# Optimization experiments

Hardware: AMD Instinct MI355X
Metric: run time of the kernel (lower is better)

The kernel has to match this reference:

```python
import jax, jax.numpy as jnp
import numpy as np

B, F, T, C = 128, 512, 60, 15  # batch, feature_size, timesteps, num_cameras
H1, H2 = 128, 64               # decoder hidden channels


def setup_inputs() -> dict:
    key = jax.random.key(0)
    ks = jax.random.split(key, 6)
    x = jax.random.normal(ks[0], (B, F, T), dtype=jnp.float32)
    cam = jax.random.randint(ks[1], (B,), 0, C)
    # per-camera (expert) decoder params
    W1 = jax.random.normal(ks[2], (C, F, H1, 3, 4), dtype=jnp.float32) * 0.02  # ConvT3d F->128, k=(1,3,4)
    b1 = jnp.zeros((C, H1), dtype=jnp.float32)
    W2 = jax.random.normal(ks[3], (C, H1, H2, 3, 4), dtype=jnp.float32) * 0.02  # ConvT3d 128->64, k=s=(1,3,4)
    b2 = jnp.zeros((C, H2), dtype=jnp.float32)
    W3 = jax.random.normal(ks[4], (C, H2), dtype=jnp.float32) * 0.02            # Conv3d 64->1, k=1
    b3 = jnp.zeros((C,), dtype=jnp.float32)
    return {"x": x, "cam": cam, "W1": W1, "b1": b1, "W2": W2, "b2": b2, "W3": W3, "b3": b3}


def reference(x, cam, W1, b1, W2, b2, W3, b3):
    # MoE-style dispatch: gather each sample's camera-expert weights.
    # Layer 1: transposed conv from 1x1 -> 3x4 is a pure linear map over features.
    h1 = jnp.einsum('bft,bfopq->btopq', x, W1[cam]) + b1[cam][:, None, :, None, None]
    h1 = jax.nn.relu(h1)                                # (B,T,128,3,4)
    # Layer 2: stride == kernel => non-overlapping transposed conv, out[3p+r,4q+s].
    h2 = jnp.einsum('btipq,biors->btoprqs', h1, W2[cam])  # (B,T,64,3,3,4,4)
    h2 = h2.reshape(B, T, H2, 9, 16) + b2[cam][:, None, :, None, None]
    h2 = jax.nn.relu(h2)                                # (B,T,64,9,16)
    # Layer 3: 1x1x1 conv to a single channel, then squeeze + sigmoid.
    out = jnp.einsum('btohw,bo->bthw', h2, W3[cam]) + b3[cam][:, None, None, None]
    return jax.nn.sigmoid(out)                           # (B,T,9,16)
```

## Files before the change

kernel.cpp:

```cpp
#include <hip/hip_runtime.h>
#include <hip/hip_bf16.h>
#include <cstdint>

#define B_  128
#define F_  512
#define T_  60
#define C_  15
#define H1_ 128
#define H2_ 64

typedef short short8_t __attribute__((ext_vector_type(8)));
typedef float f32x4    __attribute__((ext_vector_type(4)));

static __device__ __forceinline__ unsigned short f2bf(float f) {
    union { float f; uint32_t u; } v; v.f = f;
    uint32_t r = v.u + 0x7FFF + ((v.u >> 16) & 1);
    return (unsigned short)(r >> 16);
}

static __device__ __forceinline__ void async_cp16(const unsigned short* g, unsigned short* l) {
    __builtin_amdgcn_global_load_lds(
        (const __attribute__((address_space(1))) unsigned int*)g,
        (__attribute__((address_space(3))) unsigned int*)l, 16, 0, 0);
}

__global__ __launch_bounds__(256) void prep_misc(
    const float* __restrict__ x, const float* __restrict__ W2,
    const int* __restrict__ cam,
    unsigned short* __restrict__ xTs, unsigned short* __restrict__ W2f,
    int* __restrict__ ord)
{
    __shared__ float sm[12288];
    const int blk = blockIdx.x, tid = threadIdx.x;

    if (blk < 512) {
        float (*xs)[61] = (float(*)[61])sm;
        const int f0 = (blk & 3) * 128, b = blk >> 2;
        #pragma unroll
        for (int it = 0; it < 32; ++it) {
            int idx = tid + it * 256;
            int fl = idx >> 6, t = idx & 63;
            if (t < T_) xs[fl][t] = x[((size_t)b * F_ + f0 + fl) * T_ + t];
        }
        __syncthreads();
        #pragma unroll
        for (int it = 0; it < 8; ++it) {
            int idx = tid + it * 256;
            int t = idx >> 5, f4 = (idx & 31) * 4;
            ushort4 o;
            o.x = (t < T_) ? f2bf(xs[f4 + 0][t]) : 0;
            o.y = (t < T_) ? f2bf(xs[f4 + 1][t]) : 0;
            o.z = (t < T_) ? f2bf(xs[f4 + 2][t]) : 0;
            o.w = (t < T_) ? f2bf(xs[f4 + 3][t]) : 0;
            const int f = f0 + f4;
            const int kc = f >> 6, within = f & 63;
            const int cc = (within >> 3) ^ (t & 7), half = (within >> 2) & 1;
            *(ushort4*)(xTs + (size_t)b * 32768 + kc * 4096 + t * 64 + cc * 8 + half * 4) = o;
        }
    } else if (blk < 632) {
        float (*ls)[384] = (float(*)[384])sm;
        const int id = blk - 512;
        const int i0 = (id & 3) * 32, o0 = ((id >> 2) & 1) * 32, c = id >> 3;
        #pragma unroll
        for (int it = 0; it < 12; ++it) {
            int idx = tid + it * 256;
            int il = idx / 96, r = idx - il * 96;
            float4 v = *(const float4*)(W2 + ((size_t)(c * H1_ + i0 + il)) * (H2_ * 12)
                                           + (size_t)o0 * 12 + r * 4);
            *(float4*)&ls[il][r * 4] = v;
        }
        __syncthreads();
        const int o_l = tid >> 3, i_l = (tid & 7) * 4;
        const int o  = o0 + o_l;
        const int nt = o >> 4, l15 = o & 15;
        const int lane = l15 + 16 * ((i_l >> 3) & 3);
        const int kk  = i0 >> 5;
        const int pos = i_l & 7;
        #pragma unroll
        for (int rs = 0; rs < 12; ++rs) {
            ushort4 v;
            v.x = f2bf(ls[i_l + 0][o_l * 12 + rs]);
            v.y = f2bf(ls[i_l + 1][o_l * 12 + rs]);
            v.z = f2bf(ls[i_l + 2][o_l * 12 + rs]);
            v.w = f2bf(ls[i_l + 3][o_l * 12 + rs]);
            *(ushort4*)(W2f + ((size_t)(c * 12 + rs) * 16 + nt * 4 + kk) * 512
                            + lane * 8 + pos) = v;
        }
    } else {
        int* cs = (int*)sm;
        if (tid < B_) cs[tid] = cam[tid];
        __syncthreads();
        if (tid < B_) {
            const int cb = cs[tid];
            int rank = 0;
            #pragma unroll 16
            for (int j = 0; j < B_; ++j) {
                int cj = cs[j];
                rank += (cj < cb || (cj == cb && j < tid)) ? 1 : 0;
            }
            ord[rank] = tid;
        }
    }
}

__global__ __launch_bounds__(256) void repack_w1(const float* __restrict__ W1,
                                                 unsigned short* __restrict__ W1s) {
    __shared__ float ls[32][384];
    const int f0 = blockIdx.x * 32, i0 = blockIdx.y * 32, c = blockIdx.z;
    const int tid = threadIdx.x;
    #pragma unroll
    for (int it = 0; it < 12; ++it) {
        int idx = tid + it * 256;
        int fl = idx / 96, r = idx - fl * 96;
        float4 v = *(const float4*)(W1 + ((size_t)(c * F_ + f0 + fl)) * (H1_ * 12)
                                       + (size_t)i0 * 12 + r * 4);
        *(float4*)&ls[fl][r * 4] = v;
    }
    __syncthreads();
    const int i_l = tid >> 3, f_l = (tid & 7) * 4;
    const int i = i0 + i_l, f = f0 + f_l;
    const int kc = f >> 6, within = f & 63;
    const int cc = (within >> 3) ^ (i & 7), half = (within >> 2) & 1;
    #pragma unroll
    for (int pq = 0; pq < 12; ++pq) {
        ushort4 o;
        o.x = f2bf(ls[f_l + 0][i_l * 12 + pq]);
        o.y = f2bf(ls[f_l + 1][i_l * 12 + pq]);
        o.z = f2bf(ls[f_l + 2][i_l * 12 + pq]);
        o.w = f2bf(ls[f_l + 3][i_l * 12 + pq]);
        *(ushort4*)(W1s + (size_t)(c * 12 + pq) * 65536
                        + kc * 8192 + i * 64 + cc * 8 + half * 4) = o;
    }
}

__global__ __launch_bounds__(256) void fused_all(
    const unsigned short* __restrict__ xTs, const unsigned short* __restrict__ W1s,
    const unsigned short* __restrict__ W2f, const int* __restrict__ cam,
    const int* __restrict__ ord,
    const float* __restrict__ b1, const float* __restrict__ b2,
    const float* __restrict__ W3, const float* __restrict__ b3,
    float* __restrict__ out)
{
    __shared__ __align__(16) unsigned short smem[24576];

    const int idx = blockIdx.x;
    const int swz = (idx & 7) * 192 + (idx >> 3);
    const int bpos = swz / 12, pq = swz - bpos * 12;
    const int b = ord[bpos];

    const int tid = threadIdx.x;
    const int w = tid >> 6, l = tid & 63;
    const int l15 = l & 15, g = l >> 4;
    const int c = cam[b];

    const unsigned short* xchunk = xTs + (size_t)b * 32768;
    const unsigned short* wchunk = W1s + (size_t)(c * 12 + pq) * 65536;

    #define STAGE1(kc, buf)                                                       \
        {                                                                         \
            _Pragma("unroll")                                                     \
            for (int k = 0; k < 2; ++k)                                           \
                async_cp16(xchunk + (kc) * 4096 + (w * 2 + k) * 512 + l * 8,      \
                           smem + (buf) * 12288 + (w * 2 + k) * 512 + l * 8);     \
            _Pragma("unroll")                                                     \
            for (int k = 0; k < 4; ++k)                                           \
                async_cp16(wchunk + (kc) * 8192 + (w * 4 + k) * 512 + l * 8,      \
                           smem + (buf) * 12288 + 4096 + (w * 4 + k) * 512 + l * 8); \
        }

    f32x4 acc1[4][2];
    #pragma unroll
    for (int mt = 0; mt < 4; ++mt) {
        acc1[mt][0] = (f32x4){0.f, 0.f, 0.f, 0.f};
        acc1[mt][1] = (f32x4){0.f, 0.f, 0.f, 0.f};
    }

    STAGE1(0, 0);
    STAGE1(1, 1);

    const int sxor = (l15 & 7);
    #pragma unroll
    for (int kc = 0; kc < 8; ++kc) {
        if (kc < 7) { asm volatile("s_waitcnt vmcnt(6)" ::: "memory"); }
        else        { asm volatile("s_waitcnt vmcnt(0)" ::: "memory"); }
        __builtin_amdgcn_s_barrier();
        asm volatile("" ::: "memory");

        const int base = (kc & 1) * 12288;
        #pragma unroll
        for (int kk2 = 0; kk2 < 2; ++kk2) {
            const int cc = (kk2 * 4 + g) ^ sxor;
            short8_t af[4], bf[2];
            #pragma unroll
            for (int mt = 0; mt < 4; ++mt)
                af[mt] = *(const short8_t*)(smem + base + (16 * mt + l15) * 64 + cc * 8);
            #pragma unroll
            for (int ni = 0; ni < 2; ++ni)
                bf[ni] = *(const short8_t*)(smem + base + 4096
                                            + (32 * w + 16 * ni + l15) * 64 + cc * 8);
            #pragma unroll
            for (int mt = 0; mt < 4; ++mt)
                #pragma unroll
                for (int ni = 0; ni < 2; ++ni)
                    acc1[mt][ni] = __builtin_amdgcn_mfma_f32_16x16x32_bf16(
                        af[mt], bf[ni], acc1[mt][ni], 0, 0, 0);
        }

        asm volatile("" ::: "memory");
        __builtin_amdgcn_s_barrier();
        if (kc < 6) STAGE1(kc + 2, kc & 1);
    }
    #undef STAGE1

    const unsigned short* W2base = W2f + (size_t)(c * 12 + w * 3) * 8192;
    short8_t bfr[2][4];
    #pragma unroll
    for (int kk = 0; kk < 4; ++kk)
        bfr[0][kk] = *(const short8_t*)(W2base + kk * 512 + l * 8);

    float w3v[4][4], b2v[4][4];
    #pragma unroll
    for (int nt = 0; nt < 4; ++nt)
        #pragma unroll
        for (int r = 0; r < 4; ++r) {
            w3v[nt][r] = W3[c * H2_ + nt * 16 + g * 4 + r];
            b2v[nt][r] = b2[c * H2_ + nt * 16 + g * 4 + r];
        }
    const float b3v = b3[c];
    const int p = pq >> 2, q = pq & 3;

    unsigned short* h1s = smem;
    #pragma unroll
    for (int ni = 0; ni < 2; ++ni) {
        const int i = 32 * w + 16 * ni + l15;
        const float b1v = b1[c * H1_ + i];
        #pragma unroll
        for (int mt = 0; mt < 4; ++mt)
            #pragma unroll
            for (int r = 0; r < 4; ++r) {
                float h = acc1[mt][ni][r] + b1v;
                h = h > 0.f ? h : 0.f;
                h1s[(16 * mt + 4 * g + r) * 136 + i] = f2bf(h);
            }
    }
    __syncthreads();

    short8_t a2[4][4];
    #pragma unroll
    for (int mt = 0; mt < 4; ++mt)
        #pragma unroll
        for (int kk = 0; kk < 4; ++kk)
            a2[mt][kk] = *(const short8_t*)&h1s[(16 * mt + l15) * 136 + 32 * kk + 8 * g];

    float s[4] = {0.f, 0.f, 0.f, 0.f};

    #pragma unroll
    for (int seg = 0; seg < 12; ++seg) {
        if (seg < 11) {
            const int ns = seg + 1;
            const unsigned short* nb = W2base + (ns >> 2) * 8192 + ((ns & 3) * 4) * 512;
            #pragma unroll
            for (int kk = 0; kk < 4; ++kk)
                bfr[(seg + 1) & 1][kk] = *(const short8_t*)(nb + kk * 512 + l * 8);
        }
        const int nt = seg & 3;
        #pragma unroll
        for (int mt = 0; mt < 4; ++mt) {
            f32x4 acc2 = (f32x4){0.f, 0.f, 0.f, 0.f};
            #pragma unroll
            for (int kk = 0; kk < 4; ++kk)
                acc2 = __builtin_amdgcn_mfma_f32_16x16x32_bf16(
                    bfr[seg & 1][kk], a2[mt][kk], acc2, 0, 0, 0);
            #pragma unroll
            for (int r = 0; r < 4; ++r)
                s[mt] = fmaf(w3v[nt][r], fmaxf(acc2[r] + b2v[nt][r], 0.f), s[mt]);
        }

        if (nt == 3) {
            const int rs = w * 3 + (seg >> 2);
            const int hrow = p * 3 + (rs >> 2), wcol = q * 4 + (rs & 3);
            #pragma unroll
            for (int mt = 0; mt < 4; ++mt) {
                s[mt] += __shfl_xor(s[mt], 16);
                s[mt] += __shfl_xor(s[mt], 32);
            }
            float v = (g & 1) ? ((g & 2) ? s[3] : s[1]) : ((g & 2) ? s[2] : s[0]);
            v += b3v;
            if (l < T_)
                out[(((size_t)b * T_ + l) * 9 + hrow) * 16 + wcol] =
                    1.f / (1.f + __expf(-v));
            s[0] = s[1] = s[2] = s[3] = 0.f;
        }
    }
}

__global__ __launch_bounds__(256) void fused_decoder_f32(
    const float* __restrict__ x,   const int* __restrict__ cam,
    const float* __restrict__ W1,  const float* __restrict__ b1,
    const float* __restrict__ W2,  const float* __restrict__ b2,
    const float* __restrict__ W3,  const float* __restrict__ b3,
    float* __restrict__ out)
{
    __shared__ float h1s[T_ * H1_];
    __shared__ float stage[8192];

    const int pq  = blockIdx.x;
    const int b   = blockIdx.y;
    const int p   = pq >> 2, q = pq & 3;
    const int tid = threadIdx.x;
    const int c   = cam[b];

    float* xs  = stage;
    float* w1s = stage + 2048;

    const int ig = tid & 31;
    const int tg = tid >> 5;

    float acc[8][4];
    #pragma unroll
    for (int a = 0; a < 8; ++a)
        #pragma unroll
        for (int j = 0; j < 4; ++j) acc[a][j] = 0.f;

    for (int f0 = 0; f0 < F_; f0 += 32) {
        __syncthreads();
        {
            int lane = tid & 63;
            int sub  = tid >> 6;
            if (lane < T_) {
                #pragma unroll
                for (int m = 0; m < 8; ++m) {
                    int kk = sub * 8 + m;
                    xs[kk * 64 + lane] = x[((size_t)b * F_ + f0 + kk) * T_ + lane];
                }
            }
        }
        for (int e = tid; e < 32 * H1_; e += 256) {
            int kk = e >> 7, i = e & 127;
            w1s[e] = W1[(((size_t)c * F_ + f0 + kk) * H1_ + i) * 12 + pq];
        }
        __syncthreads();
        #pragma unroll 8
        for (int kk = 0; kk < 32; ++kk) {
            float4 bv = *(const float4*)&w1s[kk * 128 + ig * 4];
            float4 a0 = *(const float4*)&xs[kk * 64 + tg * 8];
            float4 a1 = *(const float4*)&xs[kk * 64 + tg * 8 + 4];
            float at[8] = {a0.x, a0.y, a0.z, a0.w, a1.x, a1.y, a1.z, a1.w};
            #pragma unroll
            for (int tt = 0; tt < 8; ++tt) {
                acc[tt][0] = fmaf(at[tt], bv.x, acc[tt][0]);
                acc[tt][1] = fmaf(at[tt], bv.y, acc[tt][1]);
                acc[tt][2] = fmaf(at[tt], bv.z, acc[tt][2]);
                acc[tt][3] = fmaf(at[tt], bv.w, acc[tt][3]);
            }
        }
    }
    {
        float4 b1v = *(const float4*)&b1[c * H1_ + ig * 4];
        #pragma unroll
        for (int tt = 0; tt < 8; ++tt) {
            int t = tg * 8 + tt;
            if (t < T_) {
                float4 hv;
                hv.x = fmaxf(acc[tt][0] + b1v.x, 0.f);
                hv.y = fmaxf(acc[tt][1] + b1v.y, 0.f);
                hv.z = fmaxf(acc[tt][2] + b1v.z, 0.f);
                hv.w = fmaxf(acc[tt][3] + b1v.w, 0.f);
                *(float4*)&h1s[t * H1_ + ig * 4] = hv;
            }
        }
    }

    const int lane = tid & 63;
    const int wv   = tid >> 6;
    const float w3v = W3[c * H2_ + lane];
    const float b2v = b2[c * H2_ + lane];
    const float b3v = b3[c];
    float* w2s = stage;

    for (int rs = 0; rs < 12; ++rs) {
        __syncthreads();
        for (int e = tid; e < H1_ * H2_; e += 256) {
            int i = e >> 6, o = e & 63;
            w2s[e] = W2[(((size_t)c * H1_ + i) * H2_ + o) * 12 + rs];
        }
        __syncthreads();

        float acc2[15];
        #pragma unroll
        for (int j = 0; j < 15; ++j) acc2[j] = 0.f;

        for (int i = 0; i < H1_; i += 4) {
            float wa = w2s[(i + 0) * 64 + lane];
            float wb = w2s[(i + 1) * 64 + lane];
            float wc = w2s[(i + 2) * 64 + lane];
            float wd = w2s[(i + 3) * 64 + lane];
            #pragma unroll
            for (int j = 0; j < 15; ++j) {
                float4 h = *(const float4*)&h1s[(wv * 15 + j) * H1_ + i];
                acc2[j] = fmaf(h.x, wa, acc2[j]);
                acc2[j] = fmaf(h.y, wb, acc2[j]);
                acc2[j] = fmaf(h.z, wc, acc2[j]);
                acc2[j] = fmaf(h.w, wd, acc2[j]);
            }
        }

        const int r = rs >> 2, s = rs & 3;
        const int hrow = p * 3 + r, wcol = q * 4 + s;
        #pragma unroll
        for (int j = 0; j < 15; ++j) {
            float y = w3v * fmaxf(acc2[j] + b2v, 0.f);
            #pragma unroll
            for (int m = 32; m > 0; m >>= 1) y += __shfl_xor(y, m, 64);
            if (lane == j) {
                int t = wv * 15 + j;
                float v = y + b3v;
                out[(((size_t)b * T_ + t) * 9 + hrow) * 16 + wcol] = 1.f / (1.f + __expf(-v));
            }
        }
    }
}

extern "C" void kernel_launch(void* const* d_in, const int* in_sizes, int n_in,
                              void* d_out, int out_size, void* d_ws, size_t ws_size,
                              hipStream_t stream) {
    const float* x   = (const float*)d_in[0];
    const int*   cam = (const int*)  d_in[1];
    const float* W1  = (const float*)d_in[2];
    const float* b1  = (const float*)d_in[3];
    const float* W2  = (const float*)d_in[4];
    const float* b2  = (const float*)d_in[5];
    const float* W3  = (const float*)d_in[6];
    const float* b3  = (const float*)d_in[7];
    float* outp = (float*)d_out;

    const size_t n_xT  = (size_t)B_ * 32768;
    const size_t n_w1s = (size_t)C_ * 12 * 65536;
    const size_t n_w2f = (size_t)C_ * 12 * 16 * 512;
    const size_t needed = (n_xT + n_w1s + n_w2f) * sizeof(unsigned short)
                        + B_ * sizeof(int);

    if (d_ws != nullptr && ws_size >= needed) {
        unsigned short* xTs = (unsigned short*)d_ws;
        unsigned short* W1p = xTs + n_xT;
        unsigned short* W2p = W1p + n_w1s;
        int* ord = (int*)(W2p + n_w2f);
        prep_misc<<<633, 256, 0, stream>>>(x, W2, cam, xTs, W2p, ord);
        repack_w1<<<dim3(F_ / 32, H1_ / 32, C_), 256, 0, stream>>>(W1, W1p);
        fused_all<<<dim3(12 * B_), 256, 0, stream>>>(
            xTs, W1p, W2p, cam, ord, b1, b2, W3, b3, outp);
    } else {
        fused_decoder_f32<<<dim3(12, B_), 256, 0, stream>>>(
            x, cam, W1, b1, W2, b2, W3, b3, outp);
    }
}
```

Before: 62.75 us.

## Merge W1 repack into prep kernel and use 3-stage 32-wide K pipeline

The separate W1 repack kernel is folded into the prep kernel, saving one launch. The first-layer GEMM now uses K chunks of 32 instead of 64 with a new XOR swizzle. It keeps three LDS buffers, so one barrier per iteration can be dropped, and total shared memory goes down. The price is twice as many iterations with less work each, plus an extra sync before h1 is written into the reused LDS.

```diff
diff --git a/kernel.cpp b/kernel.cpp
--- a/kernel.cpp
+++ b/kernel.cpp
@@ -24,11 +24,13 @@
         (__attribute__((address_space(3))) unsigned int*)l, 16, 0, 0);
 }
 
-__global__ __launch_bounds__(256) void prep_misc(
+#define KEY(r) (((r) & 3) ^ (((r) >> 2) & 3))
+
+__global__ __launch_bounds__(256) void prep_all(
     const float* __restrict__ x, const float* __restrict__ W2,
-    const int* __restrict__ cam,
+    const float* __restrict__ W1, const int* __restrict__ cam,
     unsigned short* __restrict__ xTs, unsigned short* __restrict__ W2f,
-    int* __restrict__ ord)
+    unsigned short* __restrict__ W1s, int* __restrict__ ord)
 {
     __shared__ float sm[12288];
     const int blk = blockIdx.x, tid = threadIdx.x;
@@ -53,9 +55,9 @@
             o.z = (t < T_) ? f2bf(xs[f4 + 2][t]) : 0;
             o.w = (t < T_) ? f2bf(xs[f4 + 3][t]) : 0;
             const int f = f0 + f4;
-            const int kc = f >> 6, within = f & 63;
-            const int cc = (within >> 3) ^ (t & 7), half = (within >> 2) & 1;
-            *(ushort4*)(xTs + (size_t)b * 32768 + kc * 4096 + t * 64 + cc * 8 + half * 4) = o;
+            const int kc = f >> 5, kl = f & 31;
+            const int cc = (kl >> 3) ^ KEY(t);
+            *(ushort4*)(xTs + (size_t)b * 32768 + kc * 2048 + t * 32 + cc * 8 + (kl & 7)) = o;
         }
     } else if (blk < 632) {
         float (*ls)[384] = (float(*)[384])sm;
@@ -86,7 +88,7 @@
             *(ushort4*)(W2f + ((size_t)(c * 12 + rs) * 16 + nt * 4 + kk) * 512
                             + lane * 8 + pos) = v;
         }
-    } else {
+    } else if (blk == 632) {
         int* cs = (int*)sm;
         if (tid < B_) cs[tid] = cam[tid];
         __syncthreads();
@@ -100,36 +102,33 @@
             }
             ord[rank] = tid;
         }
-    }
-}
-
-__global__ __launch_bounds__(256) void repack_w1(const float* __restrict__ W1,
-                                                 unsigned short* __restrict__ W1s) {
-    __shared__ float ls[32][384];
-    const int f0 = blockIdx.x * 32, i0 = blockIdx.y * 32, c = blockIdx.z;
-    const int tid = threadIdx.x;
-    #pragma unroll
-    for (int it = 0; it < 12; ++it) {
-        int idx = tid + it * 256;
-        int fl = idx / 96, r = idx - fl * 96;
-        float4 v = *(const float4*)(W1 + ((size_t)(c * F_ + f0 + fl)) * (H1_ * 12)
-                                       + (size_t)i0 * 12 + r * 4);
-        *(float4*)&ls[fl][r * 4] = v;
-    }
-    __syncthreads();
-    const int i_l = tid >> 3, f_l = (tid & 7) * 4;
-    const int i = i0 + i_l, f = f0 + f_l;
-    const int kc = f >> 6, within = f & 63;
-    const int cc = (within >> 3) ^ (i & 7), half = (within >> 2) & 1;
-    #pragma unroll
-    for (int pq = 0; pq < 12; ++pq) {
-        ushort4 o;
-        o.x = f2bf(ls[f_l + 0][i_l * 12 + pq]);
-        o.y = f2bf(ls[f_l + 1][i_l * 12 + pq]);
-        o.z = f2bf(ls[f_l + 2][i_l * 12 + pq]);
-        o.w = f2bf(ls[f_l + 3][i_l * 12 + pq]);
-        *(ushort4*)(W1s + (size_t)(c * 12 + pq) * 65536
-                        + kc * 8192 + i * 64 + cc * 8 + half * 4) = o;
+    } else {
+        float (*ls)[384] = (float(*)[384])sm;
+        const int id = blk - 633;
+        const int f0 = (id & 15) * 32, i0 = ((id >> 4) & 3) * 32, c = id >> 6;
+        #pragma unroll
+        for (int it = 0; it < 12; ++it) {
+            int idx = tid + it * 256;
+            int fl = idx / 96, r = idx - fl * 96;
+            float4 v = *(const float4*)(W1 + ((size_t)(c * F_ + f0 + fl)) * (H1_ * 12)
+                                           + (size_t)i0 * 12 + r * 4);
+            *(float4*)&ls[fl][r * 4] = v;
+        }
+        __syncthreads();
+        const int i_l = tid >> 3, f_l = (tid & 7) * 4;
+        const int i = i0 + i_l, f = f0 + f_l;
+        const int kc = f >> 5, kl = f & 31;
+        const int cc = (kl >> 3) ^ KEY(i);
+        #pragma unroll
+        for (int pq = 0; pq < 12; ++pq) {
+            ushort4 o;
+            o.x = f2bf(ls[f_l + 0][i_l * 12 + pq]);
+            o.y = f2bf(ls[f_l + 1][i_l * 12 + pq]);
+            o.z = f2bf(ls[f_l + 2][i_l * 12 + pq]);
+            o.w = f2bf(ls[f_l + 3][i_l * 12 + pq]);
+            *(ushort4*)(W1s + (size_t)(c * 12 + pq) * 65536
+                            + kc * 4096 + i * 32 + cc * 8 + (kl & 7)) = o;
+        }
     }
 }
 
@@ -141,7 +140,7 @@
     const float* __restrict__ W3, const float* __restrict__ b3,
     float* __restrict__ out)
 {
-    __shared__ __align__(16) unsigned short smem[24576];
+    __shared__ __align__(16) unsigned short smem[18432];
 
     const int idx = blockIdx.x;
     const int swz = (idx & 7) * 192 + (idx >> 3);
@@ -158,14 +157,12 @@
 
     #define STAGE1(kc, buf)                                                       \
         {                                                                         \
+            async_cp16(xchunk + (kc) * 2048 + w * 512 + l * 8,                    \
+                       smem + (buf) * 6144 + w * 512 + l * 8);                    \
             _Pragma("unroll")                                                     \
             for (int k = 0; k < 2; ++k)                                           \
-                async_cp16(xchunk + (kc) * 4096 + (w * 2 + k) * 512 + l * 8,      \
-                           smem + (buf) * 12288 + (w * 2 + k) * 512 + l * 8);     \
-            _Pragma("unroll")                                                     \
-            for (int k = 0; k < 4; ++k)                                           \
-                async_cp16(wchunk + (kc) * 8192 + (w * 4 + k) * 512 + l * 8,      \
-                           smem + (buf) * 12288 + 4096 + (w * 4 + k) * 512 + l * 8); \
+                async_cp16(wchunk + (kc) * 4096 + (w * 2 + k) * 512 + l * 8,      \
+                           smem + (buf) * 6144 + 2048 + (w * 2 + k) * 512 + l * 8); \
         }
 
     f32x4 acc1[4][2];
@@ -178,37 +175,33 @@
     STAGE1(0, 0);
     STAGE1(1, 1);
 
-    const int sxor = (l15 & 7);
-    #pragma unroll
-    for (int kc = 0; kc < 8; ++kc) {
-        if (kc < 7) { asm volatile("s_waitcnt vmcnt(6)" ::: "memory"); }
-        else        { asm volatile("s_waitcnt vmcnt(0)" ::: "memory"); }
+    const int key = (l15 & 3) ^ ((l15 >> 2) & 3);
+    const int ccr = (g ^ key) * 8;
+
+    #pragma unroll
+    for (int kc = 0; kc < 16; ++kc) {
+        if (kc < 15) { asm volatile("s_waitcnt vmcnt(3)" ::: "memory"); }
+        else         { asm volatile("s_waitcnt vmcnt(0)" ::: "memory"); }
         __builtin_amdgcn_s_barrier();
         asm volatile("" ::: "memory");
 
-        const int base = (kc & 1) * 12288;
-        #pragma unroll
-        for (int kk2 = 0; kk2 < 2; ++kk2) {
-            const int cc = (kk2 * 4 + g) ^ sxor;
-            short8_t af[4], bf[2];
-            #pragma unroll
-            for (int mt = 0; mt < 4; ++mt)
-                af[mt] = *(const short8_t*)(smem + base + (16 * mt + l15) * 64 + cc * 8);
+        const unsigned short* base = smem + (kc % 3) * 6144;
+        short8_t af[4], bf[2];
+        #pragma unroll
+        for (int mt = 0; mt < 4; ++mt)
+            af[mt] = *(const short8_t*)(base + (16 * mt + l15) * 32 + ccr);
+        #pragma unroll
+        for (int ni = 0; ni < 2; ++ni)
+            bf[ni] = *(const short8_t*)(base + 2048 + (32 * w + 16 * ni + l15) * 32 + ccr);
+        #pragma unroll
+        for (int mt = 0; mt < 4; ++mt)
             #pragma unroll
             for (int ni = 0; ni < 2; ++ni)
-                bf[ni] = *(const short8_t*)(smem + base + 4096
-                                            + (32 * w + 16 * ni + l15) * 64 + cc * 8);
-            #pragma unroll
-            for (int mt = 0; mt < 4; ++mt)
-                #pragma unroll
-                for (int ni = 0; ni < 2; ++ni)
-                    acc1[mt][ni] = __builtin_amdgcn_mfma_f32_16x16x32_bf16(
-                        af[mt], bf[ni], acc1[mt][ni], 0, 0, 0);
-        }
+                acc1[mt][ni] = __builtin_amdgcn_mfma_f32_16x16x32_bf16(
+                    af[mt], bf[ni], acc1[mt][ni], 0, 0, 0);
 
         asm volatile("" ::: "memory");
-        __builtin_amdgcn_s_barrier();
-        if (kc < 6) STAGE1(kc + 2, kc & 1);
+        if (kc < 14) STAGE1(kc + 2, (kc + 2) % 3);
     }
     #undef STAGE1
 
@@ -228,6 +221,8 @@
         }
     const float b3v = b3[c];
     const int p = pq >> 2, q = pq & 3;
+
+    __syncthreads();
 
     unsigned short* h1s = smem;
     #pragma unroll
@@ -445,8 +440,7 @@
         unsigned short* W1p = xTs + n_xT;
         unsigned short* W2p = W1p + n_w1s;
         int* ord = (int*)(W2p + n_w2f);
-        prep_misc<<<633, 256, 0, stream>>>(x, W2, cam, xTs, W2p, ord);
-        repack_w1<<<dim3(F_ / 32, H1_ / 32, C_), 256, 0, stream>>>(W1, W1p);
+        prep_all<<<1593, 256, 0, stream>>>(x, W2, W1, cam, xTs, W2p, W1p, ord);
         fused_all<<<dim3(12 * B_), 256, 0, stream>>>(
             xTs, W1p, W2p, cam, ord, b1, b2, W3, b3, outp);
     } else {
```

New measurement: 60.84 us. 1.03x faster.
